# Kernel tuning notes

Hardware: AMD Instinct MI355X
Metric: run time of the kernel (lower is better)

The kernel has to match this reference:

```python
import jax, jax.numpy as jnp
import numpy as np

B, NP1, K = 256, 10000, 32
NEG_INF = -1000000000.0


def setup_inputs() -> dict:
    key = jax.random.key(0)
    ks = jax.random.split(key, 7)
    query = jax.random.normal(ks[0], (B, 2), dtype=jnp.float32)
    psi_prime = jax.random.normal(ks[1], (B, NP1, 2), dtype=jnp.float32)
    knn_indices = jax.random.randint(ks[2], (B, NP1, K), 0, NP1, dtype=jnp.int32)
    mask = jax.random.randint(ks[3], (B, NP1), 0, 2, dtype=jnp.int32).astype(bool)
    current_coords = jax.random.uniform(ks[4], (B, 2), dtype=jnp.float32)
    all_coords = jax.random.uniform(ks[5], (B, NP1, 2), dtype=jnp.float32)
    lambda_param = jnp.float32(0.1)
    mu_param = jnp.float32(0.5)
    return {
        "query": query,
        "psi_prime": psi_prime,
        "knn_indices": knn_indices,
        "mask": mask,
        "current_coords": current_coords,
        "all_coords": all_coords,
        "lambda_param": lambda_param,
        "mu_param": mu_param,
    }


def _eknn(psi_prime, knn_indices):
    # psi_prime: [B, N+1, 2], knn_indices: [B, N+1, k] -> [B, N+1]
    b, np1, k = knn_indices.shape
    flat = knn_indices.reshape(b, np1 * k)
    neighbors = jnp.take_along_axis(psi_prime, flat[..., None], axis=1)
    neighbors = neighbors.reshape(b, np1, k, 2)
    # dot each node embedding with its k neighbor embeddings, sum over k
    return jnp.einsum("bnd,bnkd->bn", psi_prime, neighbors)


def reference(query, psi_prime, knn_indices, mask, current_coords, all_coords, lambda_param, mu_param):
    # context attention score: [B, N+1]
    context_scores = jnp.einsum("bnd,bd->bn", psi_prime, query)
    # kNN interference: [B, N+1]
    interference = _eknn(psi_prime, knn_indices)
    # euclidean distance penalty: [B, N+1]
    diff = all_coords - current_coords[:, None, :]
    dist_to_nodes = jnp.sqrt(jnp.sum(diff * diff, axis=-1))
    scores = context_scores + lambda_param * interference - mu_param * dist_to_nodes
    scores = jnp.where(mask, NEG_INF, scores)
    return jax.nn.log_softmax(scores, axis=-1)
```

## Files before the change

kernel.cpp:

```cpp
#include <hip/hip_runtime.h>

#define NB      256
#define NP1     10000
#define KNN     32
#define THREADS 1024
#define NWAVES  (THREADS / 64)
#define HALF_N  (NP1 / 2)
#define ITEMS_F 10
#define ITEMS_H 5
#define GROUPS_H (HALF_N / 8)
#define NEG_INF -1000000000.0f

__global__ __launch_bounds__(THREADS, 8) void hybrid_scores_kernel(
    const float* __restrict__ query,
    const float* __restrict__ psi,
    const int*   __restrict__ knn,
    const int*   __restrict__ mask,
    const float* __restrict__ cur,
    const float* __restrict__ allc,
    const float* __restrict__ lam_p,
    const float* __restrict__ mu_p,
    float* __restrict__ out,
    float2* __restrict__ ws_ms)
{
    __shared__ unsigned s_psi[NP1];
    __shared__ float    s_intf[HALF_N];
    __shared__ float    red[NWAVES];

    const int bid  = blockIdx.x;
    const int xcd  = bid & 7;
    const int slot = bid >> 3;
    const int b    = xcd * 32 + (slot >> 1);
    const int half = slot & 1;

    const int t    = threadIdx.x;
    const int lane = t & 63;
    const int wid  = t >> 6;
    const int nbase = half * HALF_N;

    const float lam = lam_p[0];
    const float mu  = mu_p[0];
    const float qx  = query[2*b],  qy = query[2*b+1];
    const float cx  = cur[2*b],    cy = cur[2*b+1];

    const float2* __restrict__ pb = (const float2*)(psi  + (long)b * NP1 * 2);
    const float2* __restrict__ ab = (const float2*)(allc + (long)b * NP1 * 2);
    const int4*   __restrict__ kb = (const int4*)(knn + (long)b * NP1 * KNN);
    const int*    __restrict__ mb = mask + (long)b * NP1;

    #pragma unroll
    for (int i = 0; i < ITEMS_F; ++i) {
        const int n = t + i * THREADS;
        if (n < NP1) {
            const float2 p = pb[n];
            unsigned ux = __float_as_uint(p.x);
            unsigned uy = __float_as_uint(p.y);
            ux = (ux + 0x7FFFu + ((ux >> 16) & 1u)) >> 16;
            uy = (uy + 0x7FFFu + ((uy >> 16) & 1u)) & 0xFFFF0000u;
            s_psi[n] = uy | ux;
        }
    }
    __syncthreads();

    const int gbase = half * GROUPS_H;
    #pragma unroll 2
    for (int g = gbase + wid; g < gbase + GROUPS_H; g += NWAVES) {
        const int4 id = kb[(size_t)g * 64 + lane];
        const int  n0 = g * 8 + (lane >> 3);

        const unsigned up = s_psi[n0];
        const float px = __uint_as_float(up << 16);
        const float py = __uint_as_float(up & 0xFFFF0000u);

        const unsigned u0 = s_psi[id.x];
        const unsigned u1 = s_psi[id.y];
        const unsigned u2 = s_psi[id.z];
        const unsigned u3 = s_psi[id.w];
        const float nsx = __uint_as_float(u0 << 16) + __uint_as_float(u1 << 16)
                        + __uint_as_float(u2 << 16) + __uint_as_float(u3 << 16);
        const float nsy = __uint_as_float(u0 & 0xFFFF0000u) + __uint_as_float(u1 & 0xFFFF0000u)
                        + __uint_as_float(u2 & 0xFFFF0000u) + __uint_as_float(u3 & 0xFFFF0000u);

        float dot = px * nsx + py * nsy;
        dot += __shfl_xor(dot, 1);
        dot += __shfl_xor(dot, 2);
        dot += __shfl_xor(dot, 4);
        if ((lane & 7) == 0) s_intf[n0 - nbase] = dot;
    }

    float2 pac[ITEMS_H];
    int    pmk[ITEMS_H];
    #pragma unroll
    for (int i = 0; i < ITEMS_H; ++i) {
        const int ln = t + i * THREADS;
        float2 ac = make_float2(0.f, 0.f);
        int    mk = 0;
        if (ln < HALF_N) {
            ac = ab[nbase + ln];
            mk = mb[nbase + ln];
        }
        pac[i] = ac; pmk[i] = mk;
    }
    __syncthreads();

    float sc[ITEMS_H];
    #pragma unroll
    for (int i = 0; i < ITEMS_H; ++i) {
        const int ln = t + i * THREADS;
        float v = -INFINITY;
        if (ln < HALF_N) {
            const unsigned up = s_psi[nbase + ln];
            const float px = __uint_as_float(up << 16);
            const float py = __uint_as_float(up & 0xFFFF0000u);
            const float2 ac = pac[i];
            const float dx = ac.x - cx, dy = ac.y - cy;
            const float dist = sqrtf(dx * dx + dy * dy);
            v = px * qx + py * qy + lam * s_intf[ln] - mu * dist;
            if (pmk[i] != 0) v = NEG_INF;
        }
        sc[i] = v;
    }

    float m = -INFINITY;
    #pragma unroll
    for (int i = 0; i < ITEMS_H; ++i) m = fmaxf(m, sc[i]);
    #pragma unroll
    for (int off = 32; off > 0; off >>= 1) m = fmaxf(m, __shfl_xor(m, off));
    if (lane == 0) red[wid] = m;
    __syncthreads();
    float M = red[0];
    #pragma unroll
    for (int w = 1; w < NWAVES; ++w) M = fmaxf(M, red[w]);
    __syncthreads();

    float s = 0.f;
    #pragma unroll
    for (int i = 0; i < ITEMS_H; ++i) s += __expf(sc[i] - M);
    #pragma unroll
    for (int off = 32; off > 0; off >>= 1) s += __shfl_xor(s, off);
    if (lane == 0) red[wid] = s;
    __syncthreads();
    if (t == 0) {
        float S = 0.f;
        #pragma unroll
        for (int w = 0; w < NWAVES; ++w) S += red[w];
        ws_ms[b * 2 + half] = make_float2(M, S);
    }

    #pragma unroll
    for (int i = 0; i < ITEMS_H; ++i) {
        const int ln = t + i * THREADS;
        if (ln < HALF_N) out[(long)b * NP1 + nbase + ln] = sc[i];
    }
}

#define CHUNK 1250
__global__ __launch_bounds__(THREADS) void hybrid_finalize_kernel(
    float* __restrict__ out, const float2* __restrict__ ws_ms)
{
    const int bid = blockIdx.x;
    const int xcd = bid & 7;
    const int k   = bid >> 3;
    const int b   = xcd * 32 + (k >> 3);
    const int cnk = k & 7;
    const int t   = threadIdx.x;

    const float2 a = ws_ms[b * 2 + 0];
    const float2 c = ws_ms[b * 2 + 1];
    const float M = fmaxf(a.x, c.x);
    const float S = a.y * __expf(a.x - M) + c.y * __expf(c.x - M);
    const float lse = M + logf(S);

    const long base = (long)b * NP1 + (long)cnk * CHUNK;
    #pragma unroll
    for (int i = 0; i < 2; ++i) {
        const int ln = t + i * THREADS;
        if (ln < CHUNK) {
            const float v = out[base + ln] - lse;
            __builtin_nontemporal_store(v, &out[base + ln]);
        }
    }
}

extern "C" void kernel_launch(void* const* d_in, const int* in_sizes, int n_in,
                              void* d_out, int out_size, void* d_ws, size_t ws_size,
                              hipStream_t stream) {
    const float* query = (const float*)d_in[0];
    const float* psi   = (const float*)d_in[1];
    const int*   knn   = (const int*)d_in[2];
    const int*   mask  = (const int*)d_in[3];
    const float* cur   = (const float*)d_in[4];
    const float* allc  = (const float*)d_in[5];
    const float* lam   = (const float*)d_in[6];
    const float* mu    = (const float*)d_in[7];
    float* out = (float*)d_out;
    float2* ws_ms = (float2*)d_ws;

    hybrid_scores_kernel<<<NB * 2, THREADS, 0, stream>>>(
        query, psi, knn, mask, cur, allc, lam, mu, out, ws_ms);
    hybrid_finalize_kernel<<<NB * 8, THREADS, 0, stream>>>(out, ws_ms);
}
```

Before: 81.19 us.

## Fuse score epilogue into kNN gather loop and stream knn with nontemporal loads

The final score computation (distance, context dot, mask, store to out) moves into the kNN gather loop and runs on one lane per node group. Scores go to shared memory for the max/sum reductions, replacing the separate coordinate/mask prefetch and score pass. The knn index loads become nontemporal, and the unroll-2 pragma is removed. In exchange, the per-node global loads and stores are now scattered and issued by only 1 of 8 lanes, which makes them less coalesced.

```diff
diff --git a/kernel.cpp b/kernel.cpp
--- a/kernel.cpp
+++ b/kernel.cpp
@@ -1,4 +1,6 @@
 #include <hip/hip_runtime.h>
+
+typedef int   int4v   __attribute__((ext_vector_type(4)));
 
 #define NB      256
 #define NP1     10000
@@ -24,7 +26,7 @@
     float2* __restrict__ ws_ms)
 {
     __shared__ unsigned s_psi[NP1];
-    __shared__ float    s_intf[HALF_N];
+    __shared__ float    s_sc[HALF_N];
     __shared__ float    red[NWAVES];
 
     const int bid  = blockIdx.x;
@@ -45,7 +47,7 @@
 
     const float2* __restrict__ pb = (const float2*)(psi  + (long)b * NP1 * 2);
     const float2* __restrict__ ab = (const float2*)(allc + (long)b * NP1 * 2);
-    const int4*   __restrict__ kb = (const int4*)(knn + (long)b * NP1 * KNN);
+    const int4v*  __restrict__ kb = (const int4v*)(knn + (long)b * NP1 * KNN);
     const int*    __restrict__ mb = mask + (long)b * NP1;
 
     #pragma unroll
@@ -63,9 +65,8 @@
     __syncthreads();
 
     const int gbase = half * GROUPS_H;
-    #pragma unroll 2
     for (int g = gbase + wid; g < gbase + GROUPS_H; g += NWAVES) {
-        const int4 id = kb[(size_t)g * 64 + lane];
+        const int4v id = __builtin_nontemporal_load(&kb[(size_t)g * 64 + lane]);
         const int  n0 = g * 8 + (lane >> 3);
 
         const unsigned up = s_psi[n0];
@@ -85,45 +86,26 @@
         dot += __shfl_xor(dot, 1);
         dot += __shfl_xor(dot, 2);
         dot += __shfl_xor(dot, 4);
-        if ((lane & 7) == 0) s_intf[n0 - nbase] = dot;
+
+        if ((lane & 7) == 0) {
+            const float2 ac = ab[n0];
+            const int    mk = mb[n0];
+            const float dx = ac.x - cx, dy = ac.y - cy;
+            const float dist = sqrtf(dx * dx + dy * dy);
+            float v = px * qx + py * qy + lam * dot - mu * dist;
+            if (mk != 0) v = NEG_INF;
+            out[(long)b * NP1 + n0] = v;
+            s_sc[n0 - nbase] = v;
+        }
     }
+    __syncthreads();
 
-    float2 pac[ITEMS_H];
-    int    pmk[ITEMS_H];
+    float m = -INFINITY;
     #pragma unroll
     for (int i = 0; i < ITEMS_H; ++i) {
         const int ln = t + i * THREADS;
-        float2 ac = make_float2(0.f, 0.f);
-        int    mk = 0;
-        if (ln < HALF_N) {
-            ac = ab[nbase + ln];
-            mk = mb[nbase + ln];
-        }
-        pac[i] = ac; pmk[i] = mk;
+        if (ln < HALF_N) m = fmaxf(m, s_sc[ln]);
     }
-    __syncthreads();
-
-    float sc[ITEMS_H];
-    #pragma unroll
-    for (int i = 0; i < ITEMS_H; ++i) {
-        const int ln = t + i * THREADS;
-        float v = -INFINITY;
-        if (ln < HALF_N) {
-            const unsigned up = s_psi[nbase + ln];
-            const float px = __uint_as_float(up << 16);
-            const float py = __uint_as_float(up & 0xFFFF0000u);
-            const float2 ac = pac[i];
-            const float dx = ac.x - cx, dy = ac.y - cy;
-            const float dist = sqrtf(dx * dx + dy * dy);
-            v = px * qx + py * qy + lam * s_intf[ln] - mu * dist;
-            if (pmk[i] != 0) v = NEG_INF;
-        }
-        sc[i] = v;
-    }
-
-    float m = -INFINITY;
-    #pragma unroll
-    for (int i = 0; i < ITEMS_H; ++i) m = fmaxf(m, sc[i]);
     #pragma unroll
     for (int off = 32; off > 0; off >>= 1) m = fmaxf(m, __shfl_xor(m, off));
     if (lane == 0) red[wid] = m;
@@ -135,7 +117,10 @@
 
     float s = 0.f;
     #pragma unroll
-    for (int i = 0; i < ITEMS_H; ++i) s += __expf(sc[i] - M);
+    for (int i = 0; i < ITEMS_H; ++i) {
+        const int ln = t + i * THREADS;
+        if (ln < HALF_N) s += __expf(s_sc[ln] - M);
+    }
     #pragma unroll
     for (int off = 32; off > 0; off >>= 1) s += __shfl_xor(s, off);
     if (lane == 0) red[wid] = s;
@@ -145,12 +130,6 @@
         #pragma unroll
         for (int w = 0; w < NWAVES; ++w) S += red[w];
         ws_ms[b * 2 + half] = make_float2(M, S);
-    }
-
-    #pragma unroll
-    for (int i = 0; i < ITEMS_H; ++i) {
-        const int ln = t + i * THREADS;
-        if (ln < HALF_N) out[(long)b * NP1 + nbase + ln] = sc[i];
     }
 }
 
```

Result: slower. 92.55 us (+14.0%).
